# Optimization experiments

Measured on AMD Instinct MI355X. Metric: run time of the kernel, lower is better.

The kernel has to match this reference:

```python
import jax, jax.numpy as jnp
import numpy as np

D_MODEL = 1024
BLOCK_SIZE = 2048


def setup_inputs() -> dict:
    key = jax.random.key(0)
    ks = jax.random.split(key, 9)
    B, T, C = 4, 2048, D_MODEL
    s = 1.0 / np.sqrt(C)
    return {
        "x": jax.random.normal(ks[0], (B, T, C), dtype=jnp.float32),
        "Wq": jax.random.normal(ks[1], (C, C), dtype=jnp.float32) * s,
        "bq": jnp.zeros((C,), dtype=jnp.float32),
        "Wk": jax.random.normal(ks[2], (C, C), dtype=jnp.float32) * s,
        "bk": jnp.zeros((C,), dtype=jnp.float32),
        "Wv": jax.random.normal(ks[3], (C, C), dtype=jnp.float32) * s,
        "bv": jnp.zeros((C,), dtype=jnp.float32),
        "Wo": jax.random.normal(ks[4], (C, C), dtype=jnp.float32) * s,
        "bo": jnp.zeros((C,), dtype=jnp.float32),
    }


def reference(x, Wq, bq, Wk, bk, Wv, bv, Wo, bo):
    B, T, C = x.shape
    q = x @ Wq + bq
    k = x @ Wk + bk
    v = x @ Wv + bv
    # NOTE: original module never splits heads; attention is over full d_model
    score = jnp.einsum("btc,bsc->bts", q, k) / jnp.sqrt(jnp.asarray(C, x.dtype))
    causal = jnp.tril(jnp.ones((T, T), dtype=bool))
    score = jnp.where(causal, score, jnp.asarray(-jnp.inf, x.dtype))
    probs = jax.nn.softmax(score, axis=-1)
    out = jnp.einsum("bts,bsc->btc", probs, v)
    return out @ Wo + bo
```

## Files before the change

kernel.cpp:

```cpp
#include <hip/hip_runtime.h>
#include <hip/hip_bf16.h>
#include <stdint.h>


typedef __attribute__((ext_vector_type(8))) __bf16 bf16x8;
typedef __attribute__((ext_vector_type(4))) __bf16 bf16x4;
typedef __attribute__((ext_vector_type(4))) float f32x4;

#define MFMA16(A, B, C) __builtin_amdgcn_mfma_f32_16x16x32_bf16(A, B, C, 0, 0, 0)
#define BAR() asm volatile("s_barrier" ::: "memory")

#define T_SEQ 2048
#define D_MOD 1024

static __device__ __forceinline__ void gload_lds16(const void* g, void* l) {
  __builtin_amdgcn_global_load_lds(
      (const __attribute__((address_space(1))) void*)g,
      (__attribute__((address_space(3))) void*)l, 16, 0, 0);
}

__global__ void cvt_bf16_kernel(const float* __restrict__ in,
                                __bf16* __restrict__ out, int n8) {
  int i = blockIdx.x * blockDim.x + threadIdx.x;
  if (i < n8) {
    const float4* p = (const float4*)(in + (size_t)i * 8);
    float4 a = p[0], b = p[1];
    bf16x8 o;
    o[0] = (__bf16)a.x; o[1] = (__bf16)a.y; o[2] = (__bf16)a.z; o[3] = (__bf16)a.w;
    o[4] = (__bf16)b.x; o[5] = (__bf16)b.y; o[6] = (__bf16)b.z; o[7] = (__bf16)b.w;
    *(bf16x8*)(out + (size_t)i * 8) = o;
  }
}

__global__ void transpose_cvt4_kernel(const float* __restrict__ Wq,
                                      const float* __restrict__ Wk,
                                      const float* __restrict__ Wv,
                                      const float* __restrict__ Wo,
                                      __bf16* __restrict__ Wqkvt,
                                      __bf16* __restrict__ Wot) {
  __shared__ float tile[32][33];
  const int z = blockIdx.z;
  const float* W = (z == 0) ? Wq : (z == 1) ? Wk : (z == 2) ? Wv : Wo;
  __bf16* Wt = (z < 3) ? (Wqkvt + (size_t)z * 1024 * 1024) : Wot;
  int tx = threadIdx.x, ty = threadIdx.y;
  int bx = blockIdx.x * 32, by = blockIdx.y * 32;
#pragma unroll
  for (int i = 0; i < 4; i++)
    tile[ty + 8 * i][tx] = W[(size_t)(by + ty + 8 * i) * D_MOD + bx + tx];
  __syncthreads();
#pragma unroll
  for (int i = 0; i < 4; i++)
    Wt[(size_t)(bx + ty + 8 * i) * D_MOD + by + tx] = (__bf16)tile[tx][ty + 8 * i];
}

__global__ __launch_bounds__(512, 2) void qkv256_kernel(
    const __bf16* __restrict__ A, const __bf16* __restrict__ Bt,
    const float* __restrict__ bq, const float* __restrict__ bk,
    const float* __restrict__ bv, __bf16* __restrict__ Qo,
    __bf16* __restrict__ Ko, __bf16* __restrict__ Vto) {
  constexpr int NT = 32;
  __shared__ __align__(16) char lds[49152];
#define ABUF(p) (lds + (p) * 8192)
#define BBUF(p) (lds + 16384 + (p) * 16384)

  const int tid = threadIdx.x;
  const int w = tid >> 6, l = tid & 63;
  const int wr = w >> 2, wc = w & 3;
  const int cpx = gridDim.x >> 3;
  const int swz = ((int)blockIdx.x & 7) * cpx + ((int)blockIdx.x >> 3);
  const int bm = (swz / 12) * 128;
  const int bn = (swz % 12) * 256;

  const int cswz = (l & 3) ^ ((l >> 3) & 3);
  const int rlo = l & 15;
  const int xsw = (((l >> 4) ^ ((l >> 1) & 3)) << 4);
  const int srow = w * 16 + (l >> 2);

#define STAGE_A(t, p)                                                  \
  {                                                                    \
    const __bf16* g = A + (size_t)(bm + srow) * 1024 + (t) * 32 +      \
                      cswz * 8;                                        \
    gload_lds16(g, ABUF(p) + w * 1024 + l * 16);                       \
  }
#define STAGE_B(t, p)                                                  \
  {                                                                    \
    const __bf16* g0 = Bt + (size_t)(bn + srow) * 1024 + (t) * 32 +    \
                       cswz * 8;                                       \
    char* d = BBUF(p) + w * 1024 + l * 16;                             \
    gload_lds16(g0, d);                                                \
    gload_lds16(g0 + (size_t)128 * 1024, d + 8192);                    \
  }

  f32x4 acc[4][4] = {};
  STAGE_A(0, 0); STAGE_B(0, 0);
  STAGE_A(1, 1); STAGE_B(1, 1);
  asm volatile("s_waitcnt vmcnt(3)" ::: "memory");
  BAR();

  for (int t = 0; t < NT; ++t) {
    const int p = t & 1;
    bf16x8 af[4], bf[4];
#pragma unroll
    for (int i = 0; i < 4; i++)
      af[i] = *(const bf16x8*)(ABUF(p) + (wr * 64 + i * 16 + rlo) * 64 + xsw);
#pragma unroll
    for (int n = 0; n < 4; n++)
      bf[n] = *(const bf16x8*)(BBUF(p) + (wc * 64 + n * 16 + rlo) * 64 + xsw);
    asm volatile("s_waitcnt lgkmcnt(0)" ::: "memory");
    BAR();
    if (t + 2 < NT) {
      STAGE_A(t + 2, p);
      STAGE_B(t + 2, p);
    }
    __builtin_amdgcn_s_setprio(1);
#pragma unroll
    for (int i = 0; i < 4; i++)
#pragma unroll
      for (int n = 0; n < 4; n++)
        acc[i][n] = MFMA16(af[i], bf[n], acc[i][n]);
    __builtin_amdgcn_s_setprio(0);
    if (t + 2 < NT) asm volatile("s_waitcnt vmcnt(3)" ::: "memory");
    else asm volatile("s_waitcnt vmcnt(0)" ::: "memory");
    BAR();
  }

  const int l4 = (l >> 4) * 4;
  const int seg = bn >> 10;
  const int bnl = bn & 1023;
  if (seg < 2) {
    const float* bs = seg ? bk : bq;
    __bf16* os = seg ? Ko : Qo;
#pragma unroll
    for (int n4 = 0; n4 < 4; n4++) {
      int col = bnl + wc * 64 + n4 * 16 + rlo;
      float bvv = bs[col];
#pragma unroll
      for (int m = 0; m < 4; m++) {
        int rowb = bm + wr * 64 + m * 16 + l4;
#pragma unroll
        for (int r = 0; r < 4; r++)
          os[(size_t)(rowb + r) * D_MOD + col] = (__bf16)(acc[m][n4][r] + bvv);
      }
    }
  } else {
#pragma unroll
    for (int n4 = 0; n4 < 4; n4++) {
      int lcol = bnl + wc * 64 + n4 * 16 + rlo;
      float bvv = bv[lcol];
#pragma unroll
      for (int m = 0; m < 4; m++) {
        int rowb = bm + wr * 64 + m * 16 + l4;
        int zz = rowb >> 11, tt = rowb & 2047;
        bf16x4 pk;
#pragma unroll
        for (int r = 0; r < 4; r++) pk[r] = (__bf16)(acc[m][n4][r] + bvv);
        *(bf16x4*)(Vto + (size_t)zz * (D_MOD * T_SEQ) + (size_t)lcol * T_SEQ +
                   tt) = pk;
      }
    }
  }
#undef ABUF
#undef BBUF
#undef STAGE_A
#undef STAGE_B
}

template <int MG, int NG>
static __device__ __forceinline__ void mfma_quad(f32x4 (&acc)[8][4],
                                                 const bf16x8 (&aR)[4][2],
                                                 const bf16x8 (&bR)[2][2]) {
#pragma unroll
  for (int i = 0; i < 4; i++)
#pragma unroll
    for (int n = 0; n < 2; n++)
#pragma unroll
      for (int kk = 0; kk < 2; kk++)
        acc[MG * 4 + i][NG * 2 + n] =
            MFMA16(aR[i][kk], bR[n][kk], acc[MG * 4 + i][NG * 2 + n]);
}

__global__ __launch_bounds__(512, 2) void qk_kernel(
    const __bf16* __restrict__ A, const __bf16* __restrict__ Bt,
    float* __restrict__ So, size_t bsA, size_t bsB, size_t bsC) {
  constexpr int NT = 16;
  __shared__ __align__(16) char lds[131072];
#define ABUF(p, h) (lds + ((p) * 2 + (h)) * 16384)
#define BBUF(p, h) (lds + 65536 + ((p) * 2 + (h)) * 16384)

  const int tid = threadIdx.x;
  const int w = tid >> 6, l = tid & 63;
  const int wr = w >> 2, wc = w & 3;
  int x = (int)blockIdx.x;
  int ti = 0;
  while (x >= ti + 1) { x -= ti + 1; ++ti; }
  const int tj = x;
  const int bm = ti * 256, bn = tj * 256;
  const int z = blockIdx.z;
  A += (size_t)z * bsA;
  Bt += (size_t)z * bsB;

  const int grow = l >> 2;
  const int cswz = (l & 3) ^ ((l >> 3) & 3);
  const int rlo = l & 15;
  const int xsw = (((l >> 4) ^ ((l >> 1) & 3)) << 4);

#define STAGE_A(t, h)                                                       \
  {                                                                         \
    const __bf16* g = A + (size_t)(bm + (h) * 128 + w * 16 + grow) * 1024 + \
                      (t) * 64 + cswz * 8;                                  \
    char* d = ABUF((t) & 1, h) + w * 1024 + l * 16;                         \
    gload_lds16(g, d);                                                      \
    gload_lds16(g + 32, d + 8192);                                          \
  }
#define STAGE_B(t, h)                                                       \
  {                                                                         \
    const __bf16* g = Bt + (size_t)(bn + (h) * 128 + w * 16 + grow) * 1024 +\
                      (t) * 64 + cswz * 8;                                  \
    char* d = BBUF((t) & 1, h) + w * 1024 + l * 16;                         \
    gload_lds16(g, d);                                                      \
    gload_lds16(g + 32, d + 8192);                                          \
  }
#define LDA_FRAG(p, g, i, kk)                                     \
  (*(const bf16x8*)(ABUF(p, wr) + (kk) * 8192 +                   \
                    ((g) * 64 + (i) * 16 + rlo) * 64 + xsw))
#define LDB_FRAG(p, g, n, kk)                                     \
  (*(const bf16x8*)(BBUF(p, (wc >> 1)) + (kk) * 8192 +            \
                    ((wc & 1) * 64 + (g) * 32 + (n) * 16 + rlo) * 64 + xsw))

  f32x4 acc[8][4] = {};
  STAGE_A(0, 0); STAGE_A(0, 1);
  STAGE_B(0, 0); STAGE_B(0, 1);
  STAGE_A(1, 0); STAGE_A(1, 1);
  asm volatile("s_waitcnt vmcnt(4)" ::: "memory");
  BAR();

  for (int t = 0; t < NT; ++t) {
    const int p = t & 1;
    bf16x8 a[4][2], b[2][2];
#pragma unroll
    for (int i = 0; i < 4; i++) {
      a[i][0] = LDA_FRAG(p, 0, i, 0);
      a[i][1] = LDA_FRAG(p, 0, i, 1);
    }
#pragma unroll
    for (int n = 0; n < 2; n++) {
      b[n][0] = LDB_FRAG(p, 0, n, 0);
      b[n][1] = LDB_FRAG(p, 0, n, 1);
    }
    if (t + 1 < NT) STAGE_B(t + 1, 0);
    BAR();
    __builtin_amdgcn_s_setprio(1);
    mfma_quad<0, 0>(acc, a, b);
    __builtin_amdgcn_s_setprio(0);
    BAR();
    bf16x8 b2[2][2];
#pragma unroll
    for (int n = 0; n < 2; n++) {
      b2[n][0] = LDB_FRAG(p, 1, n, 0);
      b2[n][1] = LDB_FRAG(p, 1, n, 1);
    }
    if (t + 1 < NT) STAGE_B(t + 1, 1);
    BAR();
    __builtin_amdgcn_s_setprio(1);
    mfma_quad<0, 1>(acc, a, b2);
    __builtin_amdgcn_s_setprio(0);
    BAR();
#pragma unroll
    for (int i = 0; i < 4; i++) {
      a[i][0] = LDA_FRAG(p, 1, i, 0);
      a[i][1] = LDA_FRAG(p, 1, i, 1);
    }
    BAR();
    __builtin_amdgcn_s_setprio(1);
    mfma_quad<1, 1>(acc, a, b2);
    __builtin_amdgcn_s_setprio(0);
    BAR();
#pragma unroll
    for (int n = 0; n < 2; n++) {
      b[n][0] = LDB_FRAG(p, 0, n, 0);
      b[n][1] = LDB_FRAG(p, 0, n, 1);
    }
    if (t + 2 < NT) {
      STAGE_A(t + 2, 0); STAGE_A(t + 2, 1);
      BAR();
      __builtin_amdgcn_s_setprio(1);
      mfma_quad<1, 0>(acc, a, b);
      __builtin_amdgcn_s_setprio(0);
      asm volatile("s_waitcnt vmcnt(4)" ::: "memory");
      BAR();
    } else {
      BAR();
      __builtin_amdgcn_s_setprio(1);
      mfma_quad<1, 0>(acc, a, b);
      __builtin_amdgcn_s_setprio(0);
      asm volatile("s_waitcnt vmcnt(0)" ::: "memory");
      BAR();
    }
  }

  float* os = So + (size_t)z * bsC;
#pragma unroll
  for (int n4 = 0; n4 < 4; n4++) {
    int col = bn + wc * 64 + n4 * 16 + rlo;
#pragma unroll
    for (int mi = 0; mi < 8; mi++) {
      int rowb = bm + wr * 128 + mi * 16 + (l >> 4) * 4;
#pragma unroll
      for (int r = 0; r < 4; r++) {
        int row = rowb + r;
        float v = acc[mi][n4][r] * 0.03125f;
        if (col > row) v = -1e30f;
        os[(size_t)row * T_SEQ + col] = v;
      }
    }
  }
#undef ABUF
#undef BBUF
#undef STAGE_A
#undef STAGE_B
#undef LDA_FRAG
#undef LDB_FRAG
}

__global__ __launch_bounds__(512, 2) void pv_kernel(
    const __bf16* __restrict__ Ap, const __bf16* __restrict__ Btp,
    __bf16* __restrict__ Op, size_t bsA, size_t bsB, size_t bsC) {
  __shared__ __align__(16) char lds[98304];
#define ABUF(p3) (lds + (p3) * 16384)
#define BBUF(p3) (lds + 49152 + (p3) * 16384)

  const int tid = threadIdx.x;
  const int w = tid >> 6, l = tid & 63;
  const int wr = w >> 2, wc = w & 3;
  const int pid = (int)blockIdx.x >> 3;
  const int bn = ((int)blockIdx.x & 7) * 128;
  const int z = blockIdx.z;
  const __bf16* A = Ap + (size_t)z * bsA;
  const __bf16* Bt = Btp + (size_t)z * bsB;
  __bf16* O = Op + (size_t)z * bsC;

  const int grow = w * 16 + (l >> 2);
  const int cswz = (l & 3) ^ ((l >> 3) & 3);
  const int rlo = l & 15;
  const int xsw = (((l >> 4) ^ ((l >> 1) & 3)) << 4);

#define PSTAGE_A(t, p3)                                                      \
  {                                                                          \
    const __bf16* g = A + (size_t)(bm + grow) * 4096 + (t) * 64 + cswz * 8;  \
    char* d = ABUF(p3) + w * 1024 + l * 16;                                  \
    gload_lds16(g, d);                                                       \
    gload_lds16(g + 32, d + 8192);                                           \
  }
#define PSTAGE_B(t, p3)                                                      \
  {                                                                          \
    const __bf16* g = Bt + (size_t)(bn + grow) * 2048 + (t) * 64 + cswz * 8; \
    char* d = BBUF(p3) + w * 1024 + l * 16;                                  \
    gload_lds16(g, d);                                                       \
    gload_lds16(g + 32, d + 8192);                                           \
  }
#define PLDA(p3, i, kk)                                           \
  (*(const bf16x8*)(ABUF(p3) + (kk) * 8192 +                      \
                    (wr * 64 + (i) * 16 + rlo) * 64 + xsw))
#define PLDB(p3, n, kk)                                           \
  (*(const bf16x8*)(BBUF(p3) + (kk) * 8192 +                      \
                    (wc * 32 + (n) * 16 + rlo) * 64 + xsw))

#pragma unroll
  for (int seg = 0; seg < 2; ++seg) {
    const int i = seg ? (15 - pid) : pid;
    const int bm = i * 128;
    const int NT = (i + 1) * 2;
    f32x4 acc[4][2] = {};

    PSTAGE_A(0, 0); PSTAGE_B(0, 0);
    if (NT > 1) { PSTAGE_A(1, 1); PSTAGE_B(1, 1); }
    asm volatile("s_waitcnt vmcnt(4)" ::: "memory");
    BAR();

    int p = 0, pn2 = 2;
    for (int t = 0; t < NT; ++t) {
      bf16x8 af[4][2], bfv[2][2];
#pragma unroll
      for (int m = 0; m < 4; m++) {
        af[m][0] = PLDA(p, m, 0);
        af[m][1] = PLDA(p, m, 1);
      }
#pragma unroll
      for (int n = 0; n < 2; n++) {
        bfv[n][0] = PLDB(p, n, 0);
        bfv[n][1] = PLDB(p, n, 1);
      }
      if (t + 2 < NT) { PSTAGE_A(t + 2, pn2); PSTAGE_B(t + 2, pn2); }
      BAR();
      __builtin_amdgcn_s_setprio(1);
#pragma unroll
      for (int m = 0; m < 4; m++)
#pragma unroll
        for (int n = 0; n < 2; n++) {
          acc[m][n] = MFMA16(af[m][0], bfv[n][0], acc[m][n]);
          acc[m][n] = MFMA16(af[m][1], bfv[n][1], acc[m][n]);
        }
      __builtin_amdgcn_s_setprio(0);
      if (t + 2 < NT) asm volatile("s_waitcnt vmcnt(4)" ::: "memory");
      else asm volatile("s_waitcnt vmcnt(0)" ::: "memory");
      BAR();
      p = (p + 1 == 3) ? 0 : p + 1;
      pn2 = (pn2 + 1 == 3) ? 0 : pn2 + 1;
    }

#pragma unroll
    for (int n = 0; n < 2; n++) {
      int col = bn + wc * 32 + n * 16 + rlo;
#pragma unroll
      for (int m = 0; m < 4; m++) {
        int rowb = bm + wr * 64 + m * 16 + (l >> 4) * 4;
#pragma unroll
        for (int r = 0; r < 4; r++)
          O[(size_t)(rowb + r) * D_MOD + col] = (__bf16)acc[m][n][r];
      }
    }
    BAR();
  }
#undef ABUF
#undef BBUF
#undef PSTAGE_A
#undef PSTAGE_B
#undef PLDA
#undef PLDB
}

__global__ __launch_bounds__(512, 2) void oproj_kernel(
    const __bf16* __restrict__ A, const __bf16* __restrict__ Bt,
    const float* __restrict__ b0, float* __restrict__ o0) {
  constexpr int NT = 16;
  __shared__ __align__(16) char lds[147456];
#define ABUF(p3) (lds + (p3) * 16384)
#define BBUF(p3) (lds + 49152 + (p3) * 32768)

  const int tid = threadIdx.x;
  const int w = tid >> 6, l = tid & 63;
  const int wr = w >> 2, wc = w & 3;
  const int cpx = gridDim.x >> 3;
  const int swz = ((int)blockIdx.x & 7) * cpx + ((int)blockIdx.x >> 3);
  const int bm = (swz >> 2) * 128, bn = (swz & 3) * 256;

  const int grow = w * 16 + (l >> 2);
  const int cswz = (l & 3) ^ ((l >> 3) & 3);
  const int rlo = l & 15;
  const int xsw = (((l >> 4) ^ ((l >> 1) & 3)) << 4);

#define STAGE_A(t, p3)                                                       \
  {                                                                          \
    const __bf16* g = A + (size_t)(bm + grow) * 1024 + (t) * 64 + cswz * 8;  \
    char* d = ABUF(p3) + w * 1024 + l * 16;                                  \
    gload_lds16(g, d);                                                       \
    gload_lds16(g + 32, d + 8192);                                           \
  }
#define STAGE_B(t, p3)                                                       \
  {                                                                          \
    const __bf16* g = Bt + (size_t)(bn + grow) * 1024 + (t) * 64 + cswz * 8; \
    char* d = BBUF(p3) + w * 1024 + l * 16;                                  \
    gload_lds16(g, d);                                                       \
    gload_lds16(g + 32, d + 16384);                                          \
    const __bf16* g2 = g + (size_t)128 * 1024;                               \
    gload_lds16(g2, d + 8192);                                               \
    gload_lds16(g2 + 32, d + 8192 + 16384);                                  \
  }
#define LDA_FRAG(p3, i, kk)                                       \
  (*(const bf16x8*)(ABUF(p3) + (kk) * 8192 +                      \
                    (wr * 64 + (i) * 16 + rlo) * 64 + xsw))
#define LDB_FRAG(p3, n, kk)                                       \
  (*(const bf16x8*)(BBUF(p3) + (kk) * 16384 +                     \
                    (wc * 64 + (n) * 16 + rlo) * 64 + xsw))

  f32x4 acc[4][4] = {};
  STAGE_A(0, 0); STAGE_B(0, 0);
  STAGE_A(1, 1); STAGE_B(1, 1);
  asm volatile("s_waitcnt vmcnt(6)" ::: "memory");
  BAR();

  int p = 0, pn2 = 2;
  for (int t = 0; t < NT; ++t) {
    bf16x8 af[4][2], bf01[2][2], bf23[2][2];
#pragma unroll
    for (int i = 0; i < 4; i++) {
      af[i][0] = LDA_FRAG(p, i, 0);
      af[i][1] = LDA_FRAG(p, i, 1);
    }
#pragma unroll
    for (int n = 0; n < 2; n++) {
      bf01[n][0] = LDB_FRAG(p, n, 0);
      bf01[n][1] = LDB_FRAG(p, n, 1);
    }
    if (t + 2 < NT) STAGE_A(t + 2, pn2);
    BAR();
    __builtin_amdgcn_s_setprio(1);
#pragma unroll
    for (int i = 0; i < 4; i++)
#pragma unroll
      for (int n = 0; n < 2; n++) {
        acc[i][n] = MFMA16(af[i][0], bf01[n][0], acc[i][n]);
        acc[i][n] = MFMA16(af[i][1], bf01[n][1], acc[i][n]);
      }
    __builtin_amdgcn_s_setprio(0);
    BAR();
#pragma unroll
    for (int n = 0; n < 2; n++) {
      bf23[n][0] = LDB_FRAG(p, n + 2, 0);
      bf23[n][1] = LDB_FRAG(p, n + 2, 1);
    }
    if (t + 2 < NT) STAGE_B(t + 2, pn2);
    BAR();
    __builtin_amdgcn_s_setprio(1);
#pragma unroll
    for (int i = 0; i < 4; i++)
#pragma unroll
      for (int n = 0; n < 2; n++) {
        acc[i][n + 2] = MFMA16(af[i][0], bf23[n][0], acc[i][n + 2]);
        acc[i][n + 2] = MFMA16(af[i][1], bf23[n][1], acc[i][n + 2]);
      }
    __builtin_amdgcn_s_setprio(0);
    if (t + 2 < NT) {
      asm volatile("s_waitcnt vmcnt(6)" ::: "memory");
    } else {
      asm volatile("s_waitcnt vmcnt(0)" ::: "memory");
    }
    BAR();
    p = (p + 1 == 3) ? 0 : p + 1;
    pn2 = (pn2 + 1 == 3) ? 0 : pn2 + 1;
  }

#pragma unroll
  for (int n = 0; n < 4; n++) {
    int col = bn + wc * 64 + n * 16 + rlo;
    float bvv = b0[col];
#pragma unroll
    for (int m = 0; m < 4; m++) {
      int rowb = bm + wr * 64 + m * 16 + (l >> 4) * 4;
#pragma unroll
      for (int r = 0; r < 4; r++)
        o0[(size_t)(rowb + r) * D_MOD + col] = acc[m][n][r] + bvv;
    }
  }
#undef ABUF
#undef BBUF
#undef STAGE_A
#undef STAGE_B
#undef LDA_FRAG
#undef LDB_FRAG
}

__global__ __launch_bounds__(256) void softmax_kernel(float* __restrict__ S,
                                                      size_t bstride) {
  const int t = blockIdx.x, b = blockIdx.y;
  float* Srow = S + (size_t)b * bstride + (size_t)t * T_SEQ;
  __bf16* Prow = (__bf16*)Srow;
  const int L = ((t + 1) + 127) & ~127;
  const int tid = threadIdx.x;
  const int base = tid * 8;
  const bool act = base < L;
  float v[8];
  float m = -1e30f;
  if (act) {
    float4 a = *(const float4*)(Srow + base);
    float4 c = *(const float4*)(Srow + base + 4);
    v[0] = a.x; v[1] = a.y; v[2] = a.z; v[3] = a.w;
    v[4] = c.x; v[5] = c.y; v[6] = c.z; v[7] = c.w;
#pragma unroll
    for (int j = 0; j < 8; j++) m = fmaxf(m, v[j]);
  }
#pragma unroll
  for (int off = 1; off < 64; off <<= 1) m = fmaxf(m, __shfl_xor(m, off));
  __shared__ float redm[4], reds[4];
  const int wave = tid >> 6, lane = tid & 63;
  if (lane == 0) redm[wave] = m;
  __syncthreads();
  m = fmaxf(fmaxf(redm[0], redm[1]), fmaxf(redm[2], redm[3]));
  float p[8];
  float s = 0.f;
  if (act) {
#pragma unroll
    for (int j = 0; j < 8; j++) {
      p[j] = __expf(v[j] - m);
      s += p[j];
    }
  }
#pragma unroll
  for (int off = 1; off < 64; off <<= 1) s += __shfl_xor(s, off);
  if (lane == 0) reds[wave] = s;
  __syncthreads();
  const float inv = 1.0f / (reds[0] + reds[1] + reds[2] + reds[3]);
  if (act) {
    bf16x8 o;
#pragma unroll
    for (int j = 0; j < 8; j++) o[j] = (__bf16)(p[j] * inv);
    *(bf16x8*)(Prow + base) = o;
  }
}

extern "C" void kernel_launch(void* const* d_in, const int* in_sizes, int n_in,
                              void* d_out, int out_size, void* d_ws,
                              size_t ws_size, hipStream_t stream) {
  const float* x = (const float*)d_in[0];
  const float* Wq = (const float*)d_in[1];
  const float* bq = (const float*)d_in[2];
  const float* Wk = (const float*)d_in[3];
  const float* bk = (const float*)d_in[4];
  const float* Wv = (const float*)d_in[5];
  const float* bv = (const float*)d_in[6];
  const float* Wo = (const float*)d_in[7];
  const float* bo = (const float*)d_in[8];

  char* ws = (char*)d_ws;
  const size_t MB = 1u << 20;
  const size_t TC = (size_t)T_SEQ * D_MOD;
  const size_t TT = (size_t)T_SEQ * T_SEQ;
  __bf16* xb    = (__bf16*)(ws);
  __bf16* Wqkvt = (__bf16*)(ws + 16 * MB);
  __bf16* Wot   = (__bf16*)(ws + 22 * MB);
  __bf16* Qb    = (__bf16*)(ws + 24 * MB);
  __bf16* Kb    = (__bf16*)(ws + 40 * MB);
  __bf16* Vtb   = (__bf16*)(ws + 56 * MB);

  cvt_bf16_kernel<<<4096, 256, 0, stream>>>(x, xb, 8192 * D_MOD / 8);
  transpose_cvt4_kernel<<<dim3(32, 32, 4), dim3(32, 8), 0, stream>>>(
      Wq, Wk, Wv, Wo, Wqkvt, Wot);
  qkv256_kernel<<<768, 512, 0, stream>>>(xb, Wqkvt, bq, bk, bv, Qb, Kb, Vtb);

  const bool batched = ws_size >= 137 * MB;
  if (batched) {
    float* S = (float*)(ws + 72 * MB);
    __bf16* AO = Qb;
    qk_kernel<<<dim3(36, 1, 4), 512, 0, stream>>>(Qb, Kb, S, TC, TC, TT);
    softmax_kernel<<<dim3(T_SEQ, 4), 256, 0, stream>>>(S, TT);
    pv_kernel<<<dim3(64, 1, 4), 512, 0, stream>>>((const __bf16*)S, Vtb, AO,
                                                  TT * 2, TC, TC);
    oproj_kernel<<<256, 512, 0, stream>>>(AO, Wot, bo, (float*)d_out);
  } else {
    float* S = (float*)(ws);
    __bf16* AO = Qb;
    for (int b = 0; b < 4; ++b) {
      qk_kernel<<<dim3(36, 1, 1), 512, 0, stream>>>(Qb + b * TC, Kb + b * TC,
                                                    S, 0, 0, 0);
      softmax_kernel<<<dim3(T_SEQ, 1), 256, 0, stream>>>(S, 0);
      pv_kernel<<<dim3(64, 1, 1), 512, 0, stream>>>(
          (const __bf16*)S, Vtb + b * TC, AO + b * TC, 0, 0, 0);
    }
    oproj_kernel<<<256, 512, 0, stream>>>(AO, Wot, bo, (float*)d_out);
  }
}
```

Measured before the change: 171.5 us.

## Shrink QK and output-projection tiles to raise grid parallelism

Replaces the 256x256 causal QK tile kernel with a 128x256 tile kernel using a K-step of 32 and a simple double-buffered pipeline. The output projection moves from 128x256 tiles with a triple buffer to 128x128 tiles with a double buffer. Both changes launch twice as many blocks with much less LDS each, to fill more of the GPU's compute units. In exchange, each block reuses less data per tile, more global loads are issued, and the finer K-steps add barrier overhead per FLOP.

```diff
diff --git a/kernel.cpp b/kernel.cpp
--- a/kernel.cpp
+++ b/kernel.cpp
@@ -165,150 +165,95 @@
 #undef STAGE_B
 }
 
-template <int MG, int NG>
-static __device__ __forceinline__ void mfma_quad(f32x4 (&acc)[8][4],
-                                                 const bf16x8 (&aR)[4][2],
-                                                 const bf16x8 (&bR)[2][2]) {
-#pragma unroll
-  for (int i = 0; i < 4; i++)
-#pragma unroll
-    for (int n = 0; n < 2; n++)
-#pragma unroll
-      for (int kk = 0; kk < 2; kk++)
-        acc[MG * 4 + i][NG * 2 + n] =
-            MFMA16(aR[i][kk], bR[n][kk], acc[MG * 4 + i][NG * 2 + n]);
-}
-
-__global__ __launch_bounds__(512, 2) void qk_kernel(
-    const __bf16* __restrict__ A, const __bf16* __restrict__ Bt,
+__global__ __launch_bounds__(512, 2) void qk128_kernel(
+    const __bf16* __restrict__ Q, const __bf16* __restrict__ K,
     float* __restrict__ So, size_t bsA, size_t bsB, size_t bsC) {
-  constexpr int NT = 16;
-  __shared__ __align__(16) char lds[131072];
-#define ABUF(p, h) (lds + ((p) * 2 + (h)) * 16384)
-#define BBUF(p, h) (lds + 65536 + ((p) * 2 + (h)) * 16384)
+  constexpr int NT = 32;
+  __shared__ __align__(16) char lds[49152];
+#define ABUF(p) (lds + (p) * 8192)
+#define BBUF(p) (lds + 16384 + (p) * 16384)
 
   const int tid = threadIdx.x;
   const int w = tid >> 6, l = tid & 63;
   const int wr = w >> 2, wc = w & 3;
-  int x = (int)blockIdx.x;
-  int ti = 0;
-  while (x >= ti + 1) { x -= ti + 1; ++ti; }
+  int x = (int)blockIdx.x, ti = 0;
+  for (;;) {
+    int cnt = (ti >> 1) + 1;
+    if (x < cnt) break;
+    x -= cnt;
+    ++ti;
+  }
   const int tj = x;
-  const int bm = ti * 256, bn = tj * 256;
-  const int z = blockIdx.z;
-  A += (size_t)z * bsA;
-  Bt += (size_t)z * bsB;
-
-  const int grow = l >> 2;
+  const int bm = ti * 128, bn = tj * 256;
+  const int z = blockIdx.y;
+  const __bf16* A = Q + (size_t)z * bsA;
+  const __bf16* Bt = K + (size_t)z * bsB;
+
   const int cswz = (l & 3) ^ ((l >> 3) & 3);
   const int rlo = l & 15;
   const int xsw = (((l >> 4) ^ ((l >> 1) & 3)) << 4);
-
-#define STAGE_A(t, h)                                                       \
-  {                                                                         \
-    const __bf16* g = A + (size_t)(bm + (h) * 128 + w * 16 + grow) * 1024 + \
-                      (t) * 64 + cswz * 8;                                  \
-    char* d = ABUF((t) & 1, h) + w * 1024 + l * 16;                         \
-    gload_lds16(g, d);                                                      \
-    gload_lds16(g + 32, d + 8192);                                          \
-  }
-#define STAGE_B(t, h)                                                       \
-  {                                                                         \
-    const __bf16* g = Bt + (size_t)(bn + (h) * 128 + w * 16 + grow) * 1024 +\
-                      (t) * 64 + cswz * 8;                                  \
-    char* d = BBUF((t) & 1, h) + w * 1024 + l * 16;                         \
-    gload_lds16(g, d);                                                      \
-    gload_lds16(g + 32, d + 8192);                                          \
-  }
-#define LDA_FRAG(p, g, i, kk)                                     \
-  (*(const bf16x8*)(ABUF(p, wr) + (kk) * 8192 +                   \
-                    ((g) * 64 + (i) * 16 + rlo) * 64 + xsw))
-#define LDB_FRAG(p, g, n, kk)                                     \
-  (*(const bf16x8*)(BBUF(p, (wc >> 1)) + (kk) * 8192 +            \
-                    ((wc & 1) * 64 + (g) * 32 + (n) * 16 + rlo) * 64 + xsw))
-
-  f32x4 acc[8][4] = {};
-  STAGE_A(0, 0); STAGE_A(0, 1);
-  STAGE_B(0, 0); STAGE_B(0, 1);
-  STAGE_A(1, 0); STAGE_A(1, 1);
-  asm volatile("s_waitcnt vmcnt(4)" ::: "memory");
+  const int srow = w * 16 + (l >> 2);
+
+#define STAGE_A(t, p)                                                  \
+  {                                                                    \
+    const __bf16* g = A + (size_t)(bm + srow) * 1024 + (t) * 32 +      \
+                      cswz * 8;                                        \
+    gload_lds16(g, ABUF(p) + w * 1024 + l * 16);                       \
+  }
+#define STAGE_B(t, p)                                                  \
+  {                                                                    \
+    const __bf16* g0 = Bt + (size_t)(bn + srow) * 1024 + (t) * 32 +    \
+                       cswz * 8;                                       \
+    char* d = BBUF(p) + w * 1024 + l * 16;                             \
+    gload_lds16(g0, d);                                                \
+    gload_lds16(g0 + (size_t)128 * 1024, d + 8192);                    \
+  }
+
+  f32x4 acc[4][4] = {};
+  STAGE_A(0, 0); STAGE_B(0, 0);
+  STAGE_A(1, 1); STAGE_B(1, 1);
+  asm volatile("s_waitcnt vmcnt(3)" ::: "memory");
   BAR();
 
   for (int t = 0; t < NT; ++t) {
     const int p = t & 1;
-    bf16x8 a[4][2], b[2][2];
-#pragma unroll
-    for (int i = 0; i < 4; i++) {
-      a[i][0] = LDA_FRAG(p, 0, i, 0);
-      a[i][1] = LDA_FRAG(p, 0, i, 1);
-    }
-#pragma unroll
-    for (int n = 0; n < 2; n++) {
-      b[n][0] = LDB_FRAG(p, 0, n, 0);
-      b[n][1] = LDB_FRAG(p, 0, n, 1);
-    }
-    if (t + 1 < NT) STAGE_B(t + 1, 0);
-    BAR();
+    bf16x8 af[4], bf[4];
+#pragma unroll
+    for (int i = 0; i < 4; i++)
+      af[i] = *(const bf16x8*)(ABUF(p) + (wr * 64 + i * 16 + rlo) * 64 + xsw);
+#pragma unroll
+    for (int n = 0; n < 4; n++)
+      bf[n] = *(const bf16x8*)(BBUF(p) + (wc * 64 + n * 16 + rlo) * 64 + xsw);
+    asm volatile("s_waitcnt lgkmcnt(0)" ::: "memory");
+    BAR();
+    if (t + 2 < NT) {
+      STAGE_A(t + 2, p);
+      STAGE_B(t + 2, p);
+    }
     __builtin_amdgcn_s_setprio(1);
-    mfma_quad<0, 0>(acc, a, b);
+#pragma unroll
+    for (int i = 0; i < 4; i++)
+#pragma unroll
+      for (int n = 0; n < 4; n++)
+        acc[i][n] = MFMA16(af[i], bf[n], acc[i][n]);
     __builtin_amdgcn_s_setprio(0);
-    BAR();
-    bf16x8 b2[2][2];
-#pragma unroll
-    for (int n = 0; n < 2; n++) {
-      b2[n][0] = LDB_FRAG(p, 1, n, 0);
-      b2[n][1] = LDB_FRAG(p, 1, n, 1);
-    }
-    if (t + 1 < NT) STAGE_B(t + 1, 1);
-    BAR();
-    __builtin_amdgcn_s_setprio(1);
-    mfma_quad<0, 1>(acc, a, b2);
-    __builtin_amdgcn_s_setprio(0);
-    BAR();
-#pragma unroll
-    for (int i = 0; i < 4; i++) {
-      a[i][0] = LDA_FRAG(p, 1, i, 0);
-      a[i][1] = LDA_FRAG(p, 1, i, 1);
-    }
-    BAR();
-    __builtin_amdgcn_s_setprio(1);
-    mfma_quad<1, 1>(acc, a, b2);
-    __builtin_amdgcn_s_setprio(0);
-    BAR();
-#pragma unroll
-    for (int n = 0; n < 2; n++) {
-      b[n][0] = LDB_FRAG(p, 0, n, 0);
-      b[n][1] = LDB_FRAG(p, 0, n, 1);
-    }
-    if (t + 2 < NT) {
-      STAGE_A(t + 2, 0); STAGE_A(t + 2, 1);
-      BAR();
-      __builtin_amdgcn_s_setprio(1);
-      mfma_quad<1, 0>(acc, a, b);
-      __builtin_amdgcn_s_setprio(0);
-      asm volatile("s_waitcnt vmcnt(4)" ::: "memory");
-      BAR();
-    } else {
-      BAR();
-      __builtin_amdgcn_s_setprio(1);
-      mfma_quad<1, 0>(acc, a, b);
-      __builtin_amdgcn_s_setprio(0);
-      asm volatile("s_waitcnt vmcnt(0)" ::: "memory");
-      BAR();
-    }
+    if (t + 2 < NT) asm volatile("s_waitcnt vmcnt(3)" ::: "memory");
+    else asm volatile("s_waitcnt vmcnt(0)" ::: "memory");
+    BAR();
   }
 
   float* os = So + (size_t)z * bsC;
+  const int l4 = (l >> 4) * 4;
 #pragma unroll
   for (int n4 = 0; n4 < 4; n4++) {
     int col = bn + wc * 64 + n4 * 16 + rlo;
 #pragma unroll
-    for (int mi = 0; mi < 8; mi++) {
-      int rowb = bm + wr * 128 + mi * 16 + (l >> 4) * 4;
+    for (int m = 0; m < 4; m++) {
+      int rowb = bm + wr * 64 + m * 16 + l4;
 #pragma unroll
       for (int r = 0; r < 4; r++) {
         int row = rowb + r;
-        float v = acc[mi][n4][r] * 0.03125f;
+        float v = acc[m][n4][r] * 0.03125f;
         if (col > row) v = -1e30f;
         os[(size_t)row * T_SEQ + col] = v;
       }
@@ -318,8 +263,92 @@
 #undef BBUF
 #undef STAGE_A
 #undef STAGE_B
-#undef LDA_FRAG
-#undef LDB_FRAG
+}
+
+__global__ __launch_bounds__(512, 2) void oproj128_kernel(
+    const __bf16* __restrict__ A, const __bf16* __restrict__ Bt,
+    const float* __restrict__ b0, float* __restrict__ o0) {
+  constexpr int NT = 32;
+  __shared__ __align__(16) char lds[32768];
+#define ABUF(p) (lds + (p) * 8192)
+#define BBUF(p) (lds + 16384 + (p) * 8192)
+
+  const int tid = threadIdx.x;
+  const int w = tid >> 6, l = tid & 63;
+  const int wr = w >> 2, wc = w & 3;
+  const int cpx = gridDim.x >> 3;
+  const int swz = ((int)blockIdx.x & 7) * cpx + ((int)blockIdx.x >> 3);
+  const int bm = (swz >> 3) * 128;
+  const int bn = (swz & 7) * 128;
+
+  const int cswz = (l & 3) ^ ((l >> 3) & 3);
+  const int rlo = l & 15;
+  const int xsw = (((l >> 4) ^ ((l >> 1) & 3)) << 4);
+  const int srow = w * 16 + (l >> 2);
+
+#define STAGE_A(t, p)                                                  \
+  {                                                                    \
+    const __bf16* g = A + (size_t)(bm + srow) * 1024 + (t) * 32 +      \
+                      cswz * 8;                                        \
+    gload_lds16(g, ABUF(p) + w * 1024 + l * 16);                       \
+  }
+#define STAGE_B(t, p)                                                  \
+  {                                                                    \
+    const __bf16* g = Bt + (size_t)(bn + srow) * 1024 + (t) * 32 +     \
+                      cswz * 8;                                        \
+    gload_lds16(g, BBUF(p) + w * 1024 + l * 16);                       \
+  }
+
+  f32x4 acc[4][2] = {};
+  STAGE_A(0, 0); STAGE_B(0, 0);
+  STAGE_A(1, 1); STAGE_B(1, 1);
+  asm volatile("s_waitcnt vmcnt(2)" ::: "memory");
+  BAR();
+
+  for (int t = 0; t < NT; ++t) {
+    const int p = t & 1;
+    bf16x8 af[4], bf[2];
+#pragma unroll
+    for (int i = 0; i < 4; i++)
+      af[i] = *(const bf16x8*)(ABUF(p) + (wr * 64 + i * 16 + rlo) * 64 + xsw);
+#pragma unroll
+    for (int n = 0; n < 2; n++)
+      bf[n] = *(const bf16x8*)(BBUF(p) + (wc * 32 + n * 16 + rlo) * 64 + xsw);
+    asm volatile("s_waitcnt lgkmcnt(0)" ::: "memory");
+    BAR();
+    if (t + 2 < NT) {
+      STAGE_A(t + 2, p);
+      STAGE_B(t + 2, p);
+    }
+    __builtin_amdgcn_s_setprio(1);
+#pragma unroll
+    for (int i = 0; i < 4; i++)
+#pragma unroll
+      for (int n = 0; n < 2; n++)
+        acc[i][n] = MFMA16(af[i], bf[n], acc[i][n]);
+    __builtin_amdgcn_s_setprio(0);
+    if (t + 2 < NT) asm volatile("s_waitcnt vmcnt(2)" ::: "memory");
+    else asm volatile("s_waitcnt vmcnt(0)" ::: "memory");
+    BAR();
+  }
+
+  const int l4 = (l >> 4) * 4;
+#pragma unroll
+  for (int n = 0; n < 2; n++) {
+    int col = bn + wc * 32 + n * 16 + rlo;
+    float bvv = b0[col];
+#pragma unroll
+    for (int m = 0; m < 4; m++) {
+      int rowb = bm + wr * 64 + m * 16 + l4;
+#pragma unroll
+      for (int r = 0; r < 4; r++)
+        o0[(size_t)(rowb + r) * D_MOD + col] = acc[m][n][r] + bvv;
+    }
+  }
+#undef ABUF
+#undef BBUF
+#undef STAGE_A
+#undef STAGE_B
 }
 
 __global__ __launch_bounds__(512, 2) void pv_kernel(
@@ -427,127 +456,6 @@
 #undef PSTAGE_B
 #undef PLDA
 #undef PLDB
-}
-
-__global__ __launch_bounds__(512, 2) void oproj_kernel(
-    const __bf16* __restrict__ A, const __bf16* __restrict__ Bt,
-    const float* __restrict__ b0, float* __restrict__ o0) {
-  constexpr int NT = 16;
-  __shared__ __align__(16) char lds[147456];
-#define ABUF(p3) (lds + (p3) * 16384)
-#define BBUF(p3) (lds + 49152 + (p3) * 32768)
-
-  const int tid = threadIdx.x;
-  const int w = tid >> 6, l = tid & 63;
-  const int wr = w >> 2, wc = w & 3;
-  const int cpx = gridDim.x >> 3;
-  const int swz = ((int)blockIdx.x & 7) * cpx + ((int)blockIdx.x >> 3);
-  const int bm = (swz >> 2) * 128, bn = (swz & 3) * 256;
-
-  const int grow = w * 16 + (l >> 2);
-  const int cswz = (l & 3) ^ ((l >> 3) & 3);
-  const int rlo = l & 15;
-  const int xsw = (((l >> 4) ^ ((l >> 1) & 3)) << 4);
-
-#define STAGE_A(t, p3)                                                       \
-  {                                                                          \
-    const __bf16* g = A + (size_t)(bm + grow) * 1024 + (t) * 64 + cswz * 8;  \
-    char* d = ABUF(p3) + w * 1024 + l * 16;                                  \
-    gload_lds16(g, d);                                                       \
-    gload_lds16(g + 32, d + 8192);                                           \
-  }
-#define STAGE_B(t, p3)                                                       \
-  {                                                                          \
-    const __bf16* g = Bt + (size_t)(bn + grow) * 1024 + (t) * 64 + cswz * 8; \
-    char* d = BBUF(p3) + w * 1024 + l * 16;                                  \
-    gload_lds16(g, d);                                                       \
-    gload_lds16(g + 32, d + 16384);                                          \
-    const __bf16* g2 = g + (size_t)128 * 1024;                               \
-    gload_lds16(g2, d + 8192);                                               \
-    gload_lds16(g2 + 32, d + 8192 + 16384);                                  \
-  }
-#define LDA_FRAG(p3, i, kk)                                       \
-  (*(const bf16x8*)(ABUF(p3) + (kk) * 8192 +                      \
-                    (wr * 64 + (i) * 16 + rlo) * 64 + xsw))
-#define LDB_FRAG(p3, n, kk)                                       \
-  (*(const bf16x8*)(BBUF(p3) + (kk) * 16384 +                     \
-                    (wc * 64 + (n) * 16 + rlo) * 64 + xsw))
-
-  f32x4 acc[4][4] = {};
-  STAGE_A(0, 0); STAGE_B(0, 0);
-  STAGE_A(1, 1); STAGE_B(1, 1);
-  asm volatile("s_waitcnt vmcnt(6)" ::: "memory");
-  BAR();
-
-  int p = 0, pn2 = 2;
-  for (int t = 0; t < NT; ++t) {
-    bf16x8 af[4][2], bf01[2][2], bf23[2][2];
-#pragma unroll
-    for (int i = 0; i < 4; i++) {
-      af[i][0] = LDA_FRAG(p, i, 0);
-      af[i][1] = LDA_FRAG(p, i, 1);
-    }
-#pragma unroll
-    for (int n = 0; n < 2; n++) {
-      bf01[n][0] = LDB_FRAG(p, n, 0);
-      bf01[n][1] = LDB_FRAG(p, n, 1);
-    }
-    if (t + 2 < NT) STAGE_A(t + 2, pn2);
-    BAR();
-    __builtin_amdgcn_s_setprio(1);
-#pragma unroll
-    for (int i = 0; i < 4; i++)
-#pragma unroll
-      for (int n = 0; n < 2; n++) {
-        acc[i][n] = MFMA16(af[i][0], bf01[n][0], acc[i][n]);
-        acc[i][n] = MFMA16(af[i][1], bf01[n][1], acc[i][n]);
-      }
-    __builtin_amdgcn_s_setprio(0);
-    BAR();
-#pragma unroll
-    for (int n = 0; n < 2; n++) {
-      bf23[n][0] = LDB_FRAG(p, n + 2, 0);
-      bf23[n][1] = LDB_FRAG(p, n + 2, 1);
-    }
-    if (t + 2 < NT) STAGE_B(t + 2, pn2);
-    BAR();
-    __builtin_amdgcn_s_setprio(1);
-#pragma unroll
-    for (int i = 0; i < 4; i++)
-#pragma unroll
-      for (int n = 0; n < 2; n++) {
-        acc[i][n + 2] = MFMA16(af[i][0], bf23[n][0], acc[i][n + 2]);
-        acc[i][n + 2] = MFMA16(af[i][1], bf23[n][1], acc[i][n + 2]);
-      }
-    __builtin_amdgcn_s_setprio(0);
-    if (t + 2 < NT) {
-      asm volatile("s_waitcnt vmcnt(6)" ::: "memory");
-    } else {
-      asm volatile("s_waitcnt vmcnt(0)" ::: "memory");
-    }
-    BAR();
-    p = (p + 1 == 3) ? 0 : p + 1;
-    pn2 = (pn2 + 1 == 3) ? 0 : pn2 + 1;
-  }
-
-#pragma unroll
-  for (int n = 0; n < 4; n++) {
-    int col = bn + wc * 64 + n * 16 + rlo;
-    float bvv = b0[col];
-#pragma unroll
-    for (int m = 0; m < 4; m++) {
-      int rowb = bm + wr * 64 + m * 16 + (l >> 4) * 4;
-#pragma unroll
-      for (int r = 0; r < 4; r++)
-        o0[(size_t)(rowb + r) * D_MOD + col] = acc[m][n][r] + bvv;
-    }
-  }
-#undef ABUF
-#undef BBUF
-#undef STAGE_A
-#undef STAGE_B
-#undef LDA_FRAG
-#undef LDB_FRAG
 }
 
 __global__ __launch_bounds__(256) void softmax_kernel(float* __restrict__ S,
@@ -631,21 +539,21 @@
   if (batched) {
     float* S = (float*)(ws + 72 * MB);
     __bf16* AO = Qb;
-    qk_kernel<<<dim3(36, 1, 4), 512, 0, stream>>>(Qb, Kb, S, TC, TC, TT);
+    qk128_kernel<<<dim3(72, 4), 512, 0, stream>>>(Qb, Kb, S, TC, TC, TT);
     softmax_kernel<<<dim3(T_SEQ, 4), 256, 0, stream>>>(S, TT);
     pv_kernel<<<dim3(64, 1, 4), 512, 0, stream>>>((const __bf16*)S, Vtb, AO,
                                                   TT * 2, TC, TC);
-    oproj_kernel<<<256, 512, 0, stream>>>(AO, Wot, bo, (float*)d_out);
+    oproj128_kernel<<<512, 512, 0, stream>>>(AO, Wot, bo, (float*)d_out);
   } else {
     float* S = (float*)(ws);
     __bf16* AO = Qb;
     for (int b = 0; b < 4; ++b) {
-      qk_kernel<<<dim3(36, 1, 1), 512, 0, stream>>>(Qb + b * TC, Kb + b * TC,
+      qk128_kernel<<<dim3(72, 1), 512, 0, stream>>>(Qb + b * TC, Kb + b * TC,
                                                     S, 0, 0, 0);
       softmax_kernel<<<dim3(T_SEQ, 1), 256, 0, stream>>>(S, 0);
       pv_kernel<<<dim3(64, 1, 1), 512, 0, stream>>>(
           (const __bf16*)S, Vtb + b * TC, AO + b * TC, 0, 0, 0);
     }
-    oproj_kernel<<<256, 512, 0, stream>>>(AO, Wot, bo, (float*)d_out);
-  }
-}
+    oproj128_kernel<<<512, 512, 0, stream>>>(AO, Wot, bo, (float*)d_out);
+  }
+}
```

Measured after the change: 177.2 us. 3.3% more time.

## Use triple-buffered LDS in QKV GEMM to drop one barrier per k-step

Applied to the files above, without the earlier changes.

The QKV projection GEMM moves from two LDS stages to three rotating stages, with the A and B tiles of each stage packed into one buffer. The prefetch two steps ahead is now issued at the top of each iteration into the stage not being read. That removes the barrier and lgkmcnt wait that used to sit between the fragment reads and the refill, leaving one barrier per k-step. In exchange LDS use grows from 48 KB to 72 KB per block, which may reduce how many blocks fit on a CU at the requested 2 blocks per CU.

```diff
diff --git a/kernel.cpp b/kernel.cpp
--- a/kernel.cpp
+++ b/kernel.cpp
@@ -53,15 +53,14 @@
     Wt[(size_t)(bx + ty + 8 * i) * D_MOD + by + tx] = (__bf16)tile[tx][ty + 8 * i];
 }
 
-__global__ __launch_bounds__(512, 2) void qkv256_kernel(
+__global__ __launch_bounds__(512, 2) void qkv256s_kernel(
     const __bf16* __restrict__ A, const __bf16* __restrict__ Bt,
     const float* __restrict__ bq, const float* __restrict__ bk,
     const float* __restrict__ bv, __bf16* __restrict__ Qo,
     __bf16* __restrict__ Ko, __bf16* __restrict__ Vto) {
   constexpr int NT = 32;
-  __shared__ __align__(16) char lds[49152];
-#define ABUF(p) (lds + (p) * 8192)
-#define BBUF(p) (lds + 16384 + (p) * 16384)
+  __shared__ __align__(16) char lds[73728];
+#define TBUF(p) (lds + (p) * 24576)
 
   const int tid = threadIdx.x;
   const int w = tid >> 6, l = tid & 63;
@@ -76,41 +75,40 @@
   const int xsw = (((l >> 4) ^ ((l >> 1) & 3)) << 4);
   const int srow = w * 16 + (l >> 2);
 
-#define STAGE_A(t, p)                                                  \
+#define STAGE(t, p)                                                    \
   {                                                                    \
-    const __bf16* g = A + (size_t)(bm + srow) * 1024 + (t) * 32 +      \
-                      cswz * 8;                                        \
-    gload_lds16(g, ABUF(p) + w * 1024 + l * 16);                       \
-  }
-#define STAGE_B(t, p)                                                  \
-  {                                                                    \
-    const __bf16* g0 = Bt + (size_t)(bn + srow) * 1024 + (t) * 32 +    \
+    const __bf16* ga = A + (size_t)(bm + srow) * 1024 + (t) * 32 +     \
                        cswz * 8;                                       \
-    char* d = BBUF(p) + w * 1024 + l * 16;                             \
-    gload_lds16(g0, d);                                                \
-    gload_lds16(g0 + (size_t)128 * 1024, d + 8192);                    \
+    gload_lds16(ga, TBUF(p) + w * 1024 + l * 16);                      \
+    const __bf16* gb = Bt + (size_t)(bn + srow) * 1024 + (t) * 32 +    \
+                       cswz * 8;                                       \
+    char* d = TBUF(p) + 8192 + w * 1024 + l * 16;                      \
+    gload_lds16(gb, d);                                                \
+    gload_lds16(gb + (size_t)128 * 1024, d + 8192);                    \
   }
 
   f32x4 acc[4][4] = {};
-  STAGE_A(0, 0); STAGE_B(0, 0);
-  STAGE_A(1, 1); STAGE_B(1, 1);
+  STAGE(0, 0);
+  STAGE(1, 1);
   asm volatile("s_waitcnt vmcnt(3)" ::: "memory");
   BAR();
 
+  int pr = 0;
   for (int t = 0; t < NT; ++t) {
-    const int p = t & 1;
+    const int ps = (pr + 2 >= 3) ? pr - 1 : pr + 2;
+    if (t + 2 < NT) STAGE(t + 2, ps);
+    if (t + 1 < NT) asm volatile("s_waitcnt vmcnt(3)" ::: "memory");
+    else asm volatile("s_waitcnt vmcnt(0)" ::: "memory");
     bf16x8 af[4], bf[4];
-#pragma unroll
-    for (int i = 0; i < 4; i++)
-      af[i] = *(const bf16x8*)(ABUF(p) + (wr * 64 + i * 16 + rlo) * 64 + xsw);
-#pragma unroll
-    for (int n = 0; n < 4; n++)
-      bf[n] = *(const bf16x8*)(BBUF(p) + (wc * 64 + n * 16 + rlo) * 64 + xsw);
-    asm volatile("s_waitcnt lgkmcnt(0)" ::: "memory");
-    BAR();
-    if (t + 2 < NT) {
-      STAGE_A(t + 2, p);
-      STAGE_B(t + 2, p);
+    {
+      char* tb = TBUF(pr);
+#pragma unroll
+      for (int i = 0; i < 4; i++)
+        af[i] = *(const bf16x8*)(tb + (wr * 64 + i * 16 + rlo) * 64 + xsw);
+#pragma unroll
+      for (int n = 0; n < 4; n++)
+        bf[n] = *(const bf16x8*)(tb + 8192 +
+                                 (wc * 64 + n * 16 + rlo) * 64 + xsw);
     }
     __builtin_amdgcn_s_setprio(1);
 #pragma unroll
@@ -119,9 +117,8 @@
       for (int n = 0; n < 4; n++)
         acc[i][n] = MFMA16(af[i], bf[n], acc[i][n]);
     __builtin_amdgcn_s_setprio(0);
-    if (t + 2 < NT) asm volatile("s_waitcnt vmcnt(3)" ::: "memory");
-    else asm volatile("s_waitcnt vmcnt(0)" ::: "memory");
-    BAR();
+    BAR();
+    pr = (pr + 1 == 3) ? 0 : pr + 1;
   }
 
   const int l4 = (l >> 4) * 4;
@@ -159,10 +156,8 @@
       }
     }
   }
-#undef ABUF
-#undef BBUF
-#undef STAGE_A
-#undef STAGE_B
+#undef TBUF
+#undef STAGE
 }
 
 template <int MG, int NG>
@@ -625,7 +620,7 @@
   cvt_bf16_kernel<<<4096, 256, 0, stream>>>(x, xb, 8192 * D_MOD / 8);
   transpose_cvt4_kernel<<<dim3(32, 32, 4), dim3(32, 8), 0, stream>>>(
       Wq, Wk, Wv, Wo, Wqkvt, Wot);
-  qkv256_kernel<<<768, 512, 0, stream>>>(xb, Wqkvt, bq, bk, bv, Qb, Kb, Vtb);
+  qkv256s_kernel<<<768, 512, 0, stream>>>(xb, Wqkvt, bq, bk, bv, Qb, Kb, Vtb);
 
   const bool batched = ws_size >= 137 * MB;
   if (batched) {
```

Measured after the change: 170.3 us. No clear change (-0.7%).
